# Optimization experiments

Hardware: AMD Instinct MI355X
Metric: run time of the kernel (lower is better)

The kernel has to match this reference:

```python
import jax, jax.numpy as jnp
import numpy as np


def setup_inputs() -> dict:
    B, S, D, H = 4, 1024, 1024, 16
    key = jax.random.key(0)
    kq, kk, kv, kl, k1, k2, k3, k4 = jax.random.split(key, 8)
    return {
        "queries": jax.random.normal(kq, (B, S, D), dtype=jnp.float32),
        "keys": jax.random.normal(kk, (B, S, D), dtype=jnp.float32),
        "values": jax.random.normal(kv, (B, S, D), dtype=jnp.float32),
        "valid_lens": jax.random.randint(kl, (B,), 1, S + 1, dtype=jnp.int32),
        "Wq": jax.random.normal(k1, (D, D), dtype=jnp.float32) / np.sqrt(D),
        "Wk": jax.random.normal(k2, (D, D), dtype=jnp.float32) / np.sqrt(D),
        "Wv": jax.random.normal(k3, (D, D), dtype=jnp.float32) / np.sqrt(D),
        "Wo": jax.random.normal(k4, (D, D), dtype=jnp.float32) / np.sqrt(D),
        "num_heads": 16,
    }


def reference(queries, keys, values, valid_lens, Wq, Wk, Wv, Wo, num_heads):
    B, Sq, D = queries.shape
    Sk = keys.shape[1]
    H = num_heads
    dh = D // H

    def split_heads(x, W):
        # [B,S,D] @ [D,D] -> [B,H,S,dh]
        return (x @ W).reshape(B, -1, H, dh).transpose(0, 2, 1, 3)

    q = split_heads(queries, Wq)
    k = split_heads(keys, Wk)
    v = split_heads(values, Wv)

    scores = jnp.einsum("bhqd,bhkd->bhqk", q, k) / jnp.sqrt(jnp.float32(dh))
    # masked_softmax: key positions >= valid_len[b] get -1e6 before softmax
    mask = jnp.arange(Sk)[None, None, None, :] < valid_lens[:, None, None, None]
    scores = jnp.where(mask, scores, jnp.float32(-1e6))
    attn = jax.nn.softmax(scores, axis=-1)  # dropout p=0.0 -> identity

    out = jnp.einsum("bhqk,bhkd->bhqd", attn, v)
    out = out.transpose(0, 2, 1, 3).reshape(B, Sq, D)
    return out @ Wo
```

## Files before the change

### kernel.cpp

```cpp
#include <hip/hip_runtime.h>
#include <hip/hip_bf16.h>
#include <cstdint>
#include <cstddef>

typedef __bf16 bf16x8 __attribute__((ext_vector_type(8)));
typedef float  f32x4  __attribute__((ext_vector_type(4)));

template <int V> struct IC { static constexpr int value = V; };

__device__ __forceinline__ unsigned short f2bf(float f) {
    unsigned x = __float_as_uint(f);
    return (unsigned short)((x + 0x7fffu + ((x >> 16) & 1u)) >> 16);
}

__device__ __forceinline__ f32x4 mfma16(bf16x8 a, bf16x8 b, f32x4 c) {
    return __builtin_amdgcn_mfma_f32_16x16x32_bf16(a, b, c, 0, 0, 0);
}

__device__ __forceinline__ int swz(int row, int col) {
    return row * 128 + ((((col >> 3) ^ (row & 7)) << 4) | ((col & 7) << 1));
}

template <int BK>
__device__ __forceinline__ int tswz(int row, int col) {
    if constexpr (BK == 64)
        return row * 128 + ((((col >> 3) ^ (row & 7)) << 4) | ((col & 7) << 1));
    else
        return row * 64 + ((((col >> 3) ^ ((row >> 1) & 3)) << 4) | ((col & 7) << 1));
}

#define GLDS16(g, l)                                                          \
    __builtin_amdgcn_global_load_lds(                                         \
        (const __attribute__((address_space(1))) void*)(g),                   \
        (__attribute__((address_space(3))) void*)(l), 16, 0, 0)

__global__ __launch_bounds__(256) void k_cvt3(const float4* __restrict__ i0,
                                              const float4* __restrict__ i1,
                                              const float4* __restrict__ i2,
                                              ushort4* __restrict__ out,
                                              int n4,
                                              const int* __restrict__ vlen) {
    if (blockIdx.z) {
        int s = blockIdx.x & 1023, b = blockIdx.x >> 10;
        if (s >= vlen[b]) return;
    }
    int i = blockIdx.x * 256 + threadIdx.x;
    if (i >= n4) return;
    const float4* in = (blockIdx.z == 0) ? i0 : (blockIdx.z == 1) ? i1 : i2;
    float4 v = in[i];
    ushort4 o;
    o.x = f2bf(v.x); o.y = f2bf(v.y); o.z = f2bf(v.z); o.w = f2bf(v.w);
    out[(size_t)blockIdx.z * n4 + i] = o;
}

__global__ __launch_bounds__(256) void k_cvt_wt4(const float* __restrict__ W0,
                                                 const float* __restrict__ W1,
                                                 const float* __restrict__ W2,
                                                 const float* __restrict__ W3,
                                                 unsigned short* __restrict__ out,
                                                 int D) {
    __shared__ float tile[32][33];
    const float* W = (blockIdx.z == 0) ? W0 : (blockIdx.z == 1) ? W1
                    : (blockIdx.z == 2) ? W2 : W3;
    unsigned short* Wt = out + (size_t)blockIdx.z * D * D;
    int c0 = blockIdx.x * 32, r0 = blockIdx.y * 32;
    int tr = threadIdx.x >> 5, tc = threadIdx.x & 31;
#pragma unroll
    for (int i = 0; i < 4; i++)
        tile[tr + 8 * i][tc] = W[(size_t)(r0 + tr + 8 * i) * D + c0 + tc];
    __syncthreads();
#pragma unroll
    for (int i = 0; i < 4; i++)
        Wt[(size_t)(c0 + tr + 8 * i) * D + r0 + tc] = f2bf(tile[tc][tr + 8 * i]);
}

__global__ __launch_bounds__(512, 2) void k_gemm8(const unsigned short* __restrict__ A0,
                                                  const unsigned short* __restrict__ Bt0,
                                                  unsigned short* __restrict__ C0,
                                                  int M, int N, int K,
                                                  size_t aStr, size_t bStr, size_t cStr,
                                                  const int* __restrict__ vlen) {
    __shared__ unsigned short As[2][256 * 64];
    __shared__ unsigned short Bs[2][256 * 64];

    const int gxy = gridDim.x * gridDim.y;
    const int nwg = gxy * gridDim.z;
    int wgid = blockIdx.z * gxy + blockIdx.y * gridDim.x + blockIdx.x;
    int sid = (wgid & 7) * (nwg >> 3) + (wgid >> 3);
    const int bz = sid / gxy;
    int rem = sid - bz * gxy;
    const int by = rem / gridDim.x;
    const int bx = rem - by * gridDim.x;

    if (bz >= 1) {
        int srow = (by << 8) & 1023;
        int bb = (by << 8) >> 10;
        if (srow >= vlen[bb]) return;
    }

    const unsigned short* A  = A0 + (size_t)bz * aStr;
    const unsigned short* Bt = Bt0 + (size_t)bz * bStr;
    unsigned short* C = C0 + (size_t)bz * cStr;

    const int t = threadIdx.x, lane = t & 63, w = t >> 6;
    const int wr = w >> 2, wc = w & 3;
    const int l15 = lane & 15, l4 = lane >> 4;
    const int brow = by * 256, bcol = bx * 256;

    f32x4 acc[8][4];
#pragma unroll
    for (int m = 0; m < 8; m++)
#pragma unroll
        for (int n = 0; n < 4; n++) acc[m][n] = f32x4{0.f, 0.f, 0.f, 0.f};

    auto stA = [&](int buf, int kt, int h) {
#pragma unroll
        for (int j = 0; j < 2; j++) {
            int c = h * 1024 + j * 512 + t;
            int row = c >> 3, slot = c & 7;
            GLDS16(A + (size_t)(brow + row) * K + kt * 64 + ((slot ^ (row & 7)) << 3),
                   (char*)As[buf] + (size_t)(h * 1024 + j * 512 + w * 64) * 16);
        }
    };
    auto stB = [&](int buf, int kt, int h) {
#pragma unroll
        for (int j = 0; j < 2; j++) {
            int c = h * 1024 + j * 512 + t;
            int row = c >> 3, slot = c & 7;
            GLDS16(Bt + (size_t)(bcol + row) * K + kt * 64 + ((slot ^ (row & 7)) << 3),
                   (char*)Bs[buf] + (size_t)(h * 1024 + j * 512 + w * 64) * 16);
        }
    };

    bf16x8 b[4][2];

    auto phase = [&](auto BUFC, auto GC, auto RBC, auto stage, auto VMC) {
        constexpr int BUF = BUFC.value, G = GC.value, VM = VMC.value;
        constexpr bool RB = RBC.value != 0;
        bf16x8 a[2][2];
#pragma unroll
        for (int i = 0; i < 2; i++)
#pragma unroll
            for (int ks = 0; ks < 2; ks++)
                a[i][ks] = *(const bf16x8*)((const char*)As[BUF] +
                           swz(wr * 128 + (2 * G + i) * 16 + l15, ks * 32 + l4 * 8));
        if constexpr (RB) {
#pragma unroll
            for (int nf = 0; nf < 4; nf++)
#pragma unroll
                for (int ks = 0; ks < 2; ks++)
                    b[nf][ks] = *(const bf16x8*)((const char*)Bs[BUF] +
                                swz(wc * 64 + nf * 16 + l15, ks * 32 + l4 * 8));
        }
        stage();
        __builtin_amdgcn_s_barrier();
        asm volatile("s_waitcnt lgkmcnt(0)" ::: "memory");
        __builtin_amdgcn_sched_barrier(0);
        __builtin_amdgcn_s_setprio(1);
#pragma unroll
        for (int i = 0; i < 2; i++)
#pragma unroll
            for (int nf = 0; nf < 4; nf++)
#pragma unroll
                for (int ks = 0; ks < 2; ks++)
                    acc[2 * G + i][nf] = mfma16(a[i][ks], b[nf][ks], acc[2 * G + i][nf]);
        __builtin_amdgcn_s_setprio(0);
        if constexpr (VM == 0) {
            asm volatile("s_waitcnt vmcnt(0)" ::: "memory");
            __builtin_amdgcn_sched_barrier(0);
        } else if constexpr (VM > 0) {
            asm volatile("s_waitcnt vmcnt(4)" ::: "memory");
            __builtin_amdgcn_sched_barrier(0);
        }
        __builtin_amdgcn_s_barrier();
    };

    auto iter = [&](int t0, auto LASTC) {
        constexpr bool LAST = LASTC.value != 0;
        phase(IC<0>{}, IC<0>{}, IC<1>{}, [&] { stA(1, t0 + 1, 0); }, IC<-1>{});
        phase(IC<0>{}, IC<1>{}, IC<0>{}, [&] { stA(1, t0 + 1, 1); }, IC<-1>{});
        phase(IC<0>{}, IC<2>{}, IC<0>{}, [&] { if constexpr (!LAST) stB(0, t0 + 2, 0); }, IC<-1>{});
        phase(IC<0>{}, IC<3>{}, IC<0>{}, [&] { if constexpr (!LAST) stB(0, t0 + 2, 1); },
              IC<LAST ? 0 : 4>{});
        phase(IC<1>{}, IC<0>{}, IC<1>{}, [&] { if constexpr (!LAST) stA(0, t0 + 2, 0); }, IC<-1>{});
        phase(IC<1>{}, IC<1>{}, IC<0>{}, [&] { if constexpr (!LAST) stA(0, t0 + 2, 1); }, IC<-1>{});
        phase(IC<1>{}, IC<2>{}, IC<0>{}, [&] { if constexpr (!LAST) stB(1, t0 + 3, 0); }, IC<-1>{});
        phase(IC<1>{}, IC<3>{}, IC<0>{}, [&] { if constexpr (!LAST) stB(1, t0 + 3, 1); },
              IC<LAST ? -1 : 4>{});
    };

    stA(0, 0, 0); stA(0, 0, 1);
    stB(0, 0, 0); stB(0, 0, 1);
    stB(1, 1, 0); stB(1, 1, 1);
    __syncthreads();

    const int NIT = K >> 7;
    for (int it = 0; it < NIT - 1; ++it) iter(2 * it, IC<0>{});
    iter(2 * (NIT - 1), IC<1>{});

#pragma unroll
    for (int mf = 0; mf < 8; mf++)
#pragma unroll
        for (int nf = 0; nf < 4; nf++)
#pragma unroll
            for (int r = 0; r < 4; r++) {
                int row = brow + wr * 128 + mf * 16 + l4 * 4 + r;
                int col = bcol + wc * 64 + nf * 16 + l15;
                C[(size_t)row * N + col] = f2bf(acc[mf][nf][r]);
            }
}

template <int BK, int TN, typename OutT>
__global__ __launch_bounds__(256) void k_gemm_bt(const unsigned short* __restrict__ A0,
                                                 const unsigned short* __restrict__ Bt0,
                                                 OutT* __restrict__ C0,
                                                 int M, int N, int K,
                                                 size_t aStr, size_t bStr, size_t cStr) {
    constexpr int NF = TN / 32;
    constexpr int SLOTS = BK / 8;
    constexpr int RA = BK / 16;
    constexpr int RB = TN * BK / 2048;

    __shared__ unsigned short As[2][128 * BK];
    __shared__ unsigned short Bs[2][TN * BK];

    const int gxy = gridDim.x * gridDim.y;
    const int nwg = gxy * gridDim.z;
    int wgid = blockIdx.z * gxy + blockIdx.y * gridDim.x + blockIdx.x;
    int sid = (wgid & 7) * (nwg >> 3) + (wgid >> 3);
    const int bz = sid / gxy;
    int rem = sid - bz * gxy;
    const int by = rem / gridDim.x;
    const int bx = rem - by * gridDim.x;

    const unsigned short* A  = A0 + (size_t)bz * aStr;
    const unsigned short* Bt = Bt0 + (size_t)bz * bStr;
    OutT* C = C0 + (size_t)bz * cStr;

    const int t = threadIdx.x;
    const int lane = t & 63, wave = t >> 6;
    const int wr = wave >> 1, wc = wave & 1;
    const int l15 = lane & 15, l4 = lane >> 4;
    const int brow = by * 128, bcol = bx * TN;

    f32x4 zero = {0.f, 0.f, 0.f, 0.f};
    f32x4 acc[4][NF];
#pragma unroll
    for (int m = 0; m < 4; m++)
#pragma unroll
        for (int n = 0; n < NF; n++) acc[m][n] = zero;

    auto stage = [&](int buf, int k0) {
#pragma unroll
        for (int i = 0; i < RA; i++) {
            int c = t + i * 256;
            int row = c / SLOTS;
            int slot = c & (SLOTS - 1);
            int gx = (BK == 64) ? (row & 7) : ((row >> 1) & 3);
            GLDS16(A + (size_t)(brow + row) * K + k0 + (slot ^ gx) * 8,
                   (char*)As[buf] + (size_t)((wave * 64 + i * 256) * 16));
        }
#pragma unroll
        for (int i = 0; i < RB; i++) {
            int c = t + i * 256;
            int row = c / SLOTS;
            int slot = c & (SLOTS - 1);
            int gx = (BK == 64) ? (row & 7) : ((row >> 1) & 3);
            GLDS16(Bt + (size_t)(bcol + row) * K + k0 + (slot ^ gx) * 8,
                   (char*)Bs[buf] + (size_t)((wave * 64 + i * 256) * 16));
        }
    };

    auto compute = [&](int buf) {
#pragma unroll
        for (int ks = 0; ks < BK / 32; ++ks) {
            bf16x8 a[4], b[NF];
#pragma unroll
            for (int m = 0; m < 4; m++) {
                int row = wr * 64 + m * 16 + l15;
                a[m] = *(const bf16x8*)((const char*)As[buf] + tswz<BK>(row, ks * 32 + l4 * 8));
            }
#pragma unroll
            for (int n = 0; n < NF; n++) {
                int row = wc * (TN / 2) + n * 16 + l15;
                b[n] = *(const bf16x8*)((const char*)Bs[buf] + tswz<BK>(row, ks * 32 + l4 * 8));
            }
            __builtin_amdgcn_s_setprio(1);
#pragma unroll
            for (int m = 0; m < 4; m++)
#pragma unroll
                for (int n = 0; n < NF; n++)
                    acc[m][n] = mfma16(a[m], b[n], acc[m][n]);
            __builtin_amdgcn_s_setprio(0);
        }
    };

    const int NT = K / BK;
    stage(0, 0);
    __syncthreads();
    int cur = 0;
    for (int kt = 0; kt < NT - 1; ++kt) {
        stage(cur ^ 1, (kt + 1) * BK);
        compute(cur);
        __syncthreads();
        cur ^= 1;
    }
    compute(cur);

#pragma unroll
    for (int m = 0; m < 4; m++)
#pragma unroll
        for (int n = 0; n < NF; n++)
#pragma unroll
            for (int r = 0; r < 4; r++) {
                int row = brow + wr * 64 + m * 16 + l4 * 4 + r;
                int col = bcol + wc * (TN / 2) + n * 16 + l15;
                float v = acc[m][n][r];
                if constexpr (sizeof(OutT) == 2)
                    ((unsigned short*)C)[(size_t)row * N + col] = f2bf(v);
                else
                    C[(size_t)row * N + col] = v;
            }
}

__global__ __launch_bounds__(256) void k_attn(const unsigned short* __restrict__ Qp,
                                              const unsigned short* __restrict__ Kp,
                                              const unsigned short* __restrict__ Vp,
                                              const int* __restrict__ valid_lens,
                                              unsigned short* __restrict__ AO,
                                              int S, int D) {
    __shared__ unsigned short Ks[2][64 * 64];
    __shared__ unsigned short Vt[2][64 * 64];
    __shared__ unsigned short Ps[64 * 64];

    const int t = threadIdx.x, lane = t & 63, w = t >> 6;
    const int l15 = lane & 15, l4 = lane >> 4;
    const int b = blockIdx.z, h = blockIdx.y, q0 = blockIdx.x * 64;
    const int vl = valid_lens[b];
    const size_t baserow = (size_t)b * S;
    const int hcol = h * 64;
    const int vr = t >> 2, vc0 = (t & 3) * 16;

    bf16x8 aq[2];
#pragma unroll
    for (int ks = 0; ks < 2; ++ks)
        aq[ks] = *(const bf16x8*)&Qp[(baserow + q0 + w * 16 + l15) * D + hcol + ks * 32 + l4 * 8];

    f32x4 zero = {0.f, 0.f, 0.f, 0.f};
    f32x4 oacc[4];
#pragma unroll
    for (int nf = 0; nf < 4; nf++) oacc[nf] = zero;
    float m_run[4], l_run[4];
#pragma unroll
    for (int r = 0; r < 4; r++) { m_run[r] = -1e30f; l_run[r] = 0.f; }

    auto stageK = [&](int buf, int kv0) {
#pragma unroll
        for (int i = 0; i < 2; i++) {
            int c = t + i * 256;
            int row = c >> 3;
            int gcol = ((c & 7) ^ (row & 7)) * 8;
            const unsigned short* gk = Kp + (baserow + kv0 + row) * D + hcol + gcol;
            GLDS16(gk, (char*)Ks[buf] + (size_t)((w * 64 + i * 256) * 16));
        }
    };
    auto loadV = [&](int kv0, bf16x8& v0, bf16x8& v1) {
        const unsigned short* gv = Vp + (baserow + kv0 + vr) * D + hcol + vc0;
        v0 = *(const bf16x8*)gv;
        v1 = *(const bf16x8*)(gv + 8);
    };
    auto writeV = [&](int buf, bf16x8 v0, bf16x8 v1) {
#pragma unroll
        for (int i = 0; i < 8; i++) {
            union { __bf16 h; unsigned short u; } c0, c1;
            c0.h = v0[i]; c1.h = v1[i];
            *(unsigned short*)((char*)Vt[buf] + swz(vc0 + i, vr)) = c0.u;
            *(unsigned short*)((char*)Vt[buf] + swz(vc0 + 8 + i, vr)) = c1.u;
        }
    };

    const int nt = (vl + 63) >> 6;
    stageK(0, 0);
    {
        bf16x8 v0, v1;
        loadV(0, v0, v1);
        writeV(0, v0, v1);
    }

    int cur = 0;
    for (int tt = 0; tt < nt; ++tt) {
        __syncthreads();

        bf16x8 nv0, nv1;
        const bool have_next = (tt + 1) < nt;
        if (have_next) {
            stageK(cur ^ 1, (tt + 1) * 64);
            loadV((tt + 1) * 64, nv0, nv1);
        }

        const int kv0 = tt * 64;
        f32x4 sacc[4];
#pragma unroll
        for (int f = 0; f < 4; f++) {
            sacc[f] = zero;
#pragma unroll
            for (int ks = 0; ks < 2; ++ks) {
                bf16x8 bk = *(const bf16x8*)((const char*)Ks[cur] + swz(f * 16 + l15, ks * 32 + l4 * 8));
                __builtin_amdgcn_s_setprio(1);
                sacc[f] = mfma16(aq[ks], bk, sacc[f]);
                __builtin_amdgcn_s_setprio(0);
            }
        }
#pragma unroll
        for (int f = 0; f < 4; f++) {
            bool masked = (kv0 + f * 16 + l15) >= vl;
#pragma unroll
            for (int r = 0; r < 4; r++) {
                float s = sacc[f][r] * 0.125f;
                sacc[f][r] = masked ? -1e30f : s;
            }
        }
        float mx[4];
#pragma unroll
        for (int r = 0; r < 4; r++)
            mx[r] = fmaxf(fmaxf(sacc[0][r], sacc[1][r]), fmaxf(sacc[2][r], sacc[3][r]));
#pragma unroll
        for (int off = 1; off < 16; off <<= 1)
#pragma unroll
            for (int r = 0; r < 4; r++) mx[r] = fmaxf(mx[r], __shfl_xor(mx[r], off));

        float nm[4], alpha[4], rs[4];
#pragma unroll
        for (int r = 0; r < 4; r++) {
            nm[r] = fmaxf(m_run[r], mx[r]);
            alpha[r] = __expf(m_run[r] - nm[r]);
            m_run[r] = nm[r];
            rs[r] = 0.f;
        }
#pragma unroll
        for (int f = 0; f < 4; f++)
#pragma unroll
            for (int r = 0; r < 4; r++) {
                float p = __expf(sacc[f][r] - nm[r]);
                rs[r] += p;
                *(unsigned short*)((char*)Ps + swz(w * 16 + l4 * 4 + r, f * 16 + l15)) = f2bf(p);
            }
#pragma unroll
        for (int off = 1; off < 16; off <<= 1)
#pragma unroll
            for (int r = 0; r < 4; r++) rs[r] += __shfl_xor(rs[r], off);
#pragma unroll
        for (int r = 0; r < 4; r++) l_run[r] = l_run[r] * alpha[r] + rs[r];
#pragma unroll
        for (int nf = 0; nf < 4; nf++)
#pragma unroll
            for (int r = 0; r < 4; r++) oacc[nf][r] *= alpha[r];

        if (have_next) writeV(cur ^ 1, nv0, nv1);

        asm volatile("s_waitcnt lgkmcnt(0)" ::: "memory");
        __builtin_amdgcn_sched_barrier(0);

        bf16x8 ap[2];
#pragma unroll
        for (int ks = 0; ks < 2; ++ks)
            ap[ks] = *(const bf16x8*)((const char*)Ps + swz(w * 16 + l15, ks * 32 + l4 * 8));
#pragma unroll
        for (int nf = 0; nf < 4; nf++)
#pragma unroll
            for (int ks = 0; ks < 2; ++ks) {
                bf16x8 bv = *(const bf16x8*)((const char*)Vt[cur] + swz(nf * 16 + l15, ks * 32 + l4 * 8));
                __builtin_amdgcn_s_setprio(1);
                oacc[nf] = mfma16(ap[ks], bv, oacc[nf]);
                __builtin_amdgcn_s_setprio(0);
            }
        cur ^= 1;
    }

#pragma unroll
    for (int nf = 0; nf < 4; nf++)
#pragma unroll
        for (int r = 0; r < 4; r++) {
            float v = oacc[nf][r] / l_run[r];
            int row = q0 + w * 16 + l4 * 4 + r;
            AO[(baserow + row) * D + hcol + nf * 16 + l15] = f2bf(v);
        }
}

extern "C" void kernel_launch(void* const* d_in, const int* in_sizes, int n_in,
                              void* d_out, int out_size, void* d_ws, size_t ws_size,
                              hipStream_t stream) {
    const float* q  = (const float*)d_in[0];
    const float* k  = (const float*)d_in[1];
    const float* v  = (const float*)d_in[2];
    const int* vlen = (const int*)d_in[3];
    const float* Wq = (const float*)d_in[4];
    const float* Wk = (const float*)d_in[5];
    const float* Wv = (const float*)d_in[6];
    const float* Wo = (const float*)d_in[7];

    const int B = in_sizes[3];
    const int D = 1024, S = 1024, H = 16;
    const int M = B * S;
    const size_t MB = 1u << 20;

    char* ws = (char*)d_ws;
    unsigned short* X   = (unsigned short*)(ws + 0 * MB);
    unsigned short* Wt  = (unsigned short*)(ws + 24 * MB);
    unsigned short* Wto = (unsigned short*)(ws + 30 * MB);
    unsigned short* P   = (unsigned short*)(ws + 32 * MB);
    unsigned short* Qp  = P;
    unsigned short* Kp  = P + 4 * 1024 * 1024;
    unsigned short* Vp  = P + 8 * 1024 * 1024;
    unsigned short* AO  = X;

    int n4 = M * D / 4;
    k_cvt3<<<dim3(n4 / 256, 1, 3), 256, 0, stream>>>(
        (const float4*)q, (const float4*)k, (const float4*)v, (ushort4*)X, n4, vlen);
    k_cvt_wt4<<<dim3(32, 32, 4), 256, 0, stream>>>(Wq, Wk, Wv, Wo, Wt, D);

    const size_t xStr = (size_t)M * D, wStr = (size_t)D * D;
    k_gemm8<<<dim3(D / 256, M / 256, 3), 512, 0, stream>>>(
        X, Wt, P, M, D, D, xStr, wStr, xStr, vlen);

    k_attn<<<dim3(S / 64, H, B), 256, 0, stream>>>(Qp, Kp, Vp, vlen, AO, S, D);

    k_gemm_bt<64, 64, float><<<dim3(D / 64, M / 128, 1), 256, 0, stream>>>(
        AO, Wto, (float*)d_out, M, D, D, 0, 0, 0);
}
```

Baseline: 97.51 us.

## Double attention query tile per block and merge prep kernels into one launch

The attention kernel now processes 128 query rows per block instead of 64, with each wave handling two 16-row MMA fragments. Each K/V tile staged in LDS is therefore reused across twice as many queries, which halves K/V global traffic and staging per query. Separately, the activation conversion and weight transpose kernels are fused into a single launch to save one kernel launch. The cost is more registers per thread, a larger P buffer in LDS, and half as many attention blocks, which could leave the GPU underfilled (512 blocks on 256 CUs).

```diff
diff --git a/kernel.cpp b/kernel.cpp
--- a/kernel.cpp
+++ b/kernel.cpp
@@ -34,44 +34,45 @@
         (const __attribute__((address_space(1))) void*)(g),                   \
         (__attribute__((address_space(3))) void*)(l), 16, 0, 0)
 
-__global__ __launch_bounds__(256) void k_cvt3(const float4* __restrict__ i0,
+__global__ __launch_bounds__(256) void k_prep(const float4* __restrict__ i0,
                                               const float4* __restrict__ i1,
                                               const float4* __restrict__ i2,
-                                              ushort4* __restrict__ out,
-                                              int n4,
-                                              const int* __restrict__ vlen) {
-    if (blockIdx.z) {
-        int s = blockIdx.x & 1023, b = blockIdx.x >> 10;
-        if (s >= vlen[b]) return;
+                                              ushort4* __restrict__ xout,
+                                              const float* __restrict__ W0,
+                                              const float* __restrict__ W1,
+                                              const float* __restrict__ W2,
+                                              const float* __restrict__ W3,
+                                              unsigned short* __restrict__ wout,
+                                              int D, const int* __restrict__ vlen) {
+    __shared__ float tile[32][33];
+    const int bid = blockIdx.x;
+    if (bid < 12288) {
+        int z = bid >> 12, rowb = bid & 4095;
+        if (z) {
+            if ((rowb & 1023) >= vlen[rowb >> 10]) return;
+        }
+        const float4* in = (z == 0) ? i0 : (z == 1) ? i1 : i2;
+        int i = rowb * 256 + threadIdx.x;
+        float4 v = in[i];
+        ushort4 o;
+        o.x = f2bf(v.x); o.y = f2bf(v.y); o.z = f2bf(v.z); o.w = f2bf(v.w);
+        xout[(size_t)z * 1048576 + i] = o;
+    } else {
+        int wid = bid - 12288;
+        int z = wid >> 10, t2 = wid & 1023;
+        int bx = t2 & 31, by = t2 >> 5;
+        const float* W = (z == 0) ? W0 : (z == 1) ? W1 : (z == 2) ? W2 : W3;
+        unsigned short* Wt = wout + (size_t)z * D * D;
+        int c0 = bx * 32, r0 = by * 32;
+        int tr = threadIdx.x >> 5, tc = threadIdx.x & 31;
+#pragma unroll
+        for (int i = 0; i < 4; i++)
+            tile[tr + 8 * i][tc] = W[(size_t)(r0 + tr + 8 * i) * D + c0 + tc];
+        __syncthreads();
+#pragma unroll
+        for (int i = 0; i < 4; i++)
+            Wt[(size_t)(c0 + tr + 8 * i) * D + r0 + tc] = f2bf(tile[tc][tr + 8 * i]);
     }
-    int i = blockIdx.x * 256 + threadIdx.x;
-    if (i >= n4) return;
-    const float4* in = (blockIdx.z == 0) ? i0 : (blockIdx.z == 1) ? i1 : i2;
-    float4 v = in[i];
-    ushort4 o;
-    o.x = f2bf(v.x); o.y = f2bf(v.y); o.z = f2bf(v.z); o.w = f2bf(v.w);
-    out[(size_t)blockIdx.z * n4 + i] = o;
-}
-
-__global__ __launch_bounds__(256) void k_cvt_wt4(const float* __restrict__ W0,
-                                                 const float* __restrict__ W1,
-                                                 const float* __restrict__ W2,
-                                                 const float* __restrict__ W3,
-                                                 unsigned short* __restrict__ out,
-                                                 int D) {
-    __shared__ float tile[32][33];
-    const float* W = (blockIdx.z == 0) ? W0 : (blockIdx.z == 1) ? W1
-                    : (blockIdx.z == 2) ? W2 : W3;
-    unsigned short* Wt = out + (size_t)blockIdx.z * D * D;
-    int c0 = blockIdx.x * 32, r0 = blockIdx.y * 32;
-    int tr = threadIdx.x >> 5, tc = threadIdx.x & 31;
-#pragma unroll
-    for (int i = 0; i < 4; i++)
-        tile[tr + 8 * i][tc] = W[(size_t)(r0 + tr + 8 * i) * D + c0 + tc];
-    __syncthreads();
-#pragma unroll
-    for (int i = 0; i < 4; i++)
-        Wt[(size_t)(c0 + tr + 8 * i) * D + r0 + tc] = f2bf(tile[tc][tr + 8 * i]);
 }
 
 __global__ __launch_bounds__(512, 2) void k_gemm8(const unsigned short* __restrict__ A0,
@@ -331,28 +332,35 @@
                                               int S, int D) {
     __shared__ unsigned short Ks[2][64 * 64];
     __shared__ unsigned short Vt[2][64 * 64];
-    __shared__ unsigned short Ps[64 * 64];
+    __shared__ unsigned short Ps[128 * 64];
 
     const int t = threadIdx.x, lane = t & 63, w = t >> 6;
     const int l15 = lane & 15, l4 = lane >> 4;
-    const int b = blockIdx.z, h = blockIdx.y, q0 = blockIdx.x * 64;
+    const int b = blockIdx.z, h = blockIdx.y, q0 = blockIdx.x * 128;
     const int vl = valid_lens[b];
     const size_t baserow = (size_t)b * S;
     const int hcol = h * 64;
     const int vr = t >> 2, vc0 = (t & 3) * 16;
 
-    bf16x8 aq[2];
-#pragma unroll
-    for (int ks = 0; ks < 2; ++ks)
-        aq[ks] = *(const bf16x8*)&Qp[(baserow + q0 + w * 16 + l15) * D + hcol + ks * 32 + l4 * 8];
+    bf16x8 aq[2][2];
+#pragma unroll
+    for (int mf = 0; mf < 2; ++mf)
+#pragma unroll
+        for (int ks = 0; ks < 2; ++ks)
+            aq[mf][ks] = *(const bf16x8*)&Qp[(baserow + q0 + w * 32 + mf * 16 + l15) * D +
+                                            hcol + ks * 32 + l4 * 8];
 
     f32x4 zero = {0.f, 0.f, 0.f, 0.f};
-    f32x4 oacc[4];
-#pragma unroll
-    for (int nf = 0; nf < 4; nf++) oacc[nf] = zero;
-    float m_run[4], l_run[4];
-#pragma unroll
-    for (int r = 0; r < 4; r++) { m_run[r] = -1e30f; l_run[r] = 0.f; }
+    f32x4 oacc[2][4];
+#pragma unroll
+    for (int mf = 0; mf < 2; mf++)
+#pragma unroll
+        for (int nf = 0; nf < 4; nf++) oacc[mf][nf] = zero;
+    float m_run[2][4], l_run[2][4];
+#pragma unroll
+    for (int mf = 0; mf < 2; mf++)
+#pragma unroll
+        for (int r = 0; r < 4; r++) { m_run[mf][r] = -1e30f; l_run[mf][r] = 0.f; }
 
     auto stageK = [&](int buf, int kv0) {
 #pragma unroll
@@ -399,15 +407,20 @@
         }
 
         const int kv0 = tt * 64;
-        f32x4 sacc[4];
+        f32x4 sacc[2][4];
+#pragma unroll
+        for (int mf = 0; mf < 2; mf++)
+#pragma unroll
+            for (int f = 0; f < 4; f++) sacc[mf][f] = zero;
 #pragma unroll
         for (int f = 0; f < 4; f++) {
-            sacc[f] = zero;
 #pragma unroll
             for (int ks = 0; ks < 2; ++ks) {
                 bf16x8 bk = *(const bf16x8*)((const char*)Ks[cur] + swz(f * 16 + l15, ks * 32 + l4 * 8));
                 __builtin_amdgcn_s_setprio(1);
-                sacc[f] = mfma16(aq[ks], bk, sacc[f]);
+#pragma unroll
+                for (int mf = 0; mf < 2; mf++)
+                    sacc[mf][f] = mfma16(aq[mf][ks], bk, sacc[mf][f]);
                 __builtin_amdgcn_s_setprio(0);
             }
         }
@@ -415,76 +428,103 @@
         for (int f = 0; f < 4; f++) {
             bool masked = (kv0 + f * 16 + l15) >= vl;
 #pragma unroll
+            for (int mf = 0; mf < 2; mf++)
+#pragma unroll
+                for (int r = 0; r < 4; r++) {
+                    float s = sacc[mf][f][r] * 0.125f;
+                    sacc[mf][f][r] = masked ? -1e30f : s;
+                }
+        }
+        float mx[2][4];
+#pragma unroll
+        for (int mf = 0; mf < 2; mf++)
+#pragma unroll
+            for (int r = 0; r < 4; r++)
+                mx[mf][r] = fmaxf(fmaxf(sacc[mf][0][r], sacc[mf][1][r]),
+                                  fmaxf(sacc[mf][2][r], sacc[mf][3][r]));
+#pragma unroll
+        for (int off = 1; off < 16; off <<= 1)
+#pragma unroll
+            for (int mf = 0; mf < 2; mf++)
+#pragma unroll
+                for (int r = 0; r < 4; r++)
+                    mx[mf][r] = fmaxf(mx[mf][r], __shfl_xor(mx[mf][r], off));
+
+        float nm[2][4], alpha[2][4], rs[2][4];
+#pragma unroll
+        for (int mf = 0; mf < 2; mf++)
+#pragma unroll
             for (int r = 0; r < 4; r++) {
-                float s = sacc[f][r] * 0.125f;
-                sacc[f][r] = masked ? -1e30f : s;
-            }
-        }
-        float mx[4];
-#pragma unroll
-        for (int r = 0; r < 4; r++)
-            mx[r] = fmaxf(fmaxf(sacc[0][r], sacc[1][r]), fmaxf(sacc[2][r], sacc[3][r]));
+                nm[mf][r] = fmaxf(m_run[mf][r], mx[mf][r]);
+                alpha[mf][r] = __expf(m_run[mf][r] - nm[mf][r]);
+                m_run[mf][r] = nm[mf][r];
+                rs[mf][r] = 0.f;
+            }
+#pragma unroll
+        for (int mf = 0; mf < 2; mf++)
+#pragma unroll
+            for (int f = 0; f < 4; f++)
+#pragma unroll
+                for (int r = 0; r < 4; r++) {
+                    float p = __expf(sacc[mf][f][r] - nm[mf][r]);
+                    rs[mf][r] += p;
+                    *(unsigned short*)((char*)Ps +
+                        swz(w * 32 + mf * 16 + l4 * 4 + r, f * 16 + l15)) = f2bf(p);
+                }
 #pragma unroll
         for (int off = 1; off < 16; off <<= 1)
 #pragma unroll
-            for (int r = 0; r < 4; r++) mx[r] = fmaxf(mx[r], __shfl_xor(mx[r], off));
-
-        float nm[4], alpha[4], rs[4];
-#pragma unroll
-        for (int r = 0; r < 4; r++) {
-            nm[r] = fmaxf(m_run[r], mx[r]);
-            alpha[r] = __expf(m_run[r] - nm[r]);
-            m_run[r] = nm[r];
-            rs[r] = 0.f;
-        }
-#pragma unroll
-        for (int f = 0; f < 4; f++)
-#pragma unroll
-            for (int r = 0; r < 4; r++) {
-                float p = __expf(sacc[f][r] - nm[r]);
-                rs[r] += p;
-                *(unsigned short*)((char*)Ps + swz(w * 16 + l4 * 4 + r, f * 16 + l15)) = f2bf(p);
-            }
-#pragma unroll
-        for (int off = 1; off < 16; off <<= 1)
-#pragma unroll
-            for (int r = 0; r < 4; r++) rs[r] += __shfl_xor(rs[r], off);
-#pragma unroll
-        for (int r = 0; r < 4; r++) l_run[r] = l_run[r] * alpha[r] + rs[r];
-#pragma unroll
-        for (int nf = 0; nf < 4; nf++)
-#pragma unroll
-            for (int r = 0; r < 4; r++) oacc[nf][r] *= alpha[r];
+            for (int mf = 0; mf < 2; mf++)
+#pragma unroll
+                for (int r = 0; r < 4; r++) rs[mf][r] += __shfl_xor(rs[mf][r], off);
+#pragma unroll
+        for (int mf = 0; mf < 2; mf++)
+#pragma unroll
+            for (int r = 0; r < 4; r++)
+                l_run[mf][r] = l_run[mf][r] * alpha[mf][r] + rs[mf][r];
+#pragma unroll
+        for (int mf = 0; mf < 2; mf++)
+#pragma unroll
+            for (int nf = 0; nf < 4; nf++)
+#pragma unroll
+                for (int r = 0; r < 4; r++) oacc[mf][nf][r] *= alpha[mf][r];
 
         if (have_next) writeV(cur ^ 1, nv0, nv1);
 
         asm volatile("s_waitcnt lgkmcnt(0)" ::: "memory");
         __builtin_amdgcn_sched_barrier(0);
 
-        bf16x8 ap[2];
-#pragma unroll
-        for (int ks = 0; ks < 2; ++ks)
-            ap[ks] = *(const bf16x8*)((const char*)Ps + swz(w * 16 + l15, ks * 32 + l4 * 8));
+        bf16x8 ap[2][2];
+#pragma unroll
+        for (int mf = 0; mf < 2; mf++)
+#pragma unroll
+            for (int ks = 0; ks < 2; ++ks)
+                ap[mf][ks] = *(const bf16x8*)((const char*)Ps +
+                             swz(w * 32 + mf * 16 + l15, ks * 32 + l4 * 8));
 #pragma unroll
         for (int nf = 0; nf < 4; nf++)
 #pragma unroll
             for (int ks = 0; ks < 2; ++ks) {
                 bf16x8 bv = *(const bf16x8*)((const char*)Vt[cur] + swz(nf * 16 + l15, ks * 32 + l4 * 8));
                 __builtin_amdgcn_s_setprio(1);
-                oacc[nf] = mfma16(ap[ks], bv, oacc[nf]);
+#pragma unroll
+                for (int mf = 0; mf < 2; mf++)
+                    oacc[mf][nf] = mfma16(ap[mf][ks], bv, oacc[mf][nf]);
                 __builtin_amdgcn_s_setprio(0);
             }
         cur ^= 1;
     }
 
 #pragma unroll
-    for (int nf = 0; nf < 4; nf++)
-#pragma unroll
-        for (int r = 0; r < 4; r++) {
-            float v = oacc[nf][r] / l_run[r];
-            int row = q0 + w * 16 + l4 * 4 + r;
-            AO[(baserow + row) * D + hcol + nf * 16 + l15] = f2bf(v);
-        }
+    for (int mf = 0; mf < 2; mf++)
+#pragma unroll
+        for (int nf = 0; nf < 4; nf++)
+#pragma unroll
+            for (int r = 0; r < 4; r++) {
+                float v = oacc[mf][nf][r] / l_run[mf][r];
+                int row = q0 + w * 32 + mf * 16 + l4 * 4 + r;
+                AO[(baserow + row) * D + hcol + nf * 16 + l15] = f2bf(v);
+            }
 }
 
 extern "C" void kernel_launch(void* const* d_in, const int* in_sizes, int n_in,
@@ -514,16 +554,15 @@
     unsigned short* Vp  = P + 8 * 1024 * 1024;
     unsigned short* AO  = X;
 
-    int n4 = M * D / 4;
-    k_cvt3<<<dim3(n4 / 256, 1, 3), 256, 0, stream>>>(
-        (const float4*)q, (const float4*)k, (const float4*)v, (ushort4*)X, n4, vlen);
-    k_cvt_wt4<<<dim3(32, 32, 4), 256, 0, stream>>>(Wq, Wk, Wv, Wo, Wt, D);
+    k_prep<<<dim3(16384), 256, 0, stream>>>(
+        (const float4*)q, (const float4*)k, (const float4*)v, (ushort4*)X,
+        Wq, Wk, Wv, Wo, Wt, D, vlen);
 
     const size_t xStr = (size_t)M * D, wStr = (size_t)D * D;
     k_gemm8<<<dim3(D / 256, M / 256, 3), 512, 0, stream>>>(
         X, Wt, P, M, D, D, xStr, wStr, xStr, vlen);
 
-    k_attn<<<dim3(S / 64, H, B), 256, 0, stream>>>(Qp, Kp, Vp, vlen, AO, S, D);
+    k_attn<<<dim3(S / 128, H, B), 256, 0, stream>>>(Qp, Kp, Vp, vlen, AO, S, D);
 
     k_gemm_bt<64, 64, float><<<dim3(D / 64, M / 128, 1), 256, 0, stream>>>(
         AO, Wto, (float*)d_out, M, D, D, 0, 0, 0);
```

After: 102.1 us. 4.7% more time.
